# Kernel optimization log

Hardware: AMD Instinct MI355X
Metric: run time of the kernel (lower is better)

Reference implementation:

```python
import jax, jax.numpy as jnp
import numpy as np

B, T, D = 32, 1024, 512   # batch, encoder length, listener feature dim (= speller hidden)
H = 512                   # speller_hidden_dim
V = 64                    # output_class_dim
S = 128                   # max_label_len (decode steps, no teacher forcing)


def setup_inputs() -> dict:
    key = jax.random.key(0)
    ks = jax.random.split(key, 7)
    s = lambda n: 1.0 / np.sqrt(n)
    return {
        "listener_feature": jax.random.normal(ks[0], (B, T, D), jnp.float32),
        "W_ih": jax.random.normal(ks[1], (4 * H, V + H), jnp.float32) * s(V + H),
        "W_hh": jax.random.normal(ks[2], (4 * H, H), jnp.float32) * s(H),
        "b_ih": jax.random.normal(ks[3], (4 * H,), jnp.float32) * 0.01,
        "b_hh": jax.random.normal(ks[4], (4 * H,), jnp.float32) * 0.01,
        "W_out": jax.random.normal(ks[5], (V, 2 * H), jnp.float32) * s(2 * H),
        "b_out": jax.random.normal(ks[6], (V,), jnp.float32) * 0.01,
    }


def reference(listener_feature, W_ih, W_hh, b_ih, b_hh, W_out, b_out):
    Bb = listener_feature.shape[0]

    def step(carry, _):
        h, c, x = carry                              # h,c: [B,H]; x: [B,V+H]
        gates = x @ W_ih.T + b_ih + h @ W_hh.T + b_hh  # [B,4H], torch gate order i,f,g,o
        i, f, g, o = jnp.split(gates, 4, axis=-1)
        i = jax.nn.sigmoid(i); f = jax.nn.sigmoid(f)
        g = jnp.tanh(g);       o = jax.nn.sigmoid(o)
        c = f * c + i * g
        h = o * jnp.tanh(c)                          # rnn_output [B,H]
        # dot attention over listener features
        energy = jnp.einsum('bd,btd->bt', h, listener_feature)   # [B,T]
        attn = jax.nn.softmax(energy, axis=-1)
        ctx = jnp.einsum('bt,btd->bd', attn, listener_feature)   # [B,D]
        concat = jnp.concatenate([h, ctx], axis=-1)              # [B,2H]
        logp = jax.nn.log_softmax(concat @ W_out.T + b_out, axis=-1)  # [B,V]
        # decode_mode == 1: greedy one-hot feedback (non-differentiable argmax)
        ow = jax.nn.one_hot(jnp.argmax(logp, axis=-1), V, dtype=logp.dtype)
        x_next = jnp.concatenate([ow, ctx], axis=-1)
        return (h, c, x_next), (logp, attn)

    # initial word = one-hot of class 0; first rnn input concatenates listener_feature[:,0,:]
    ow0 = jnp.zeros((Bb, V), listener_feature.dtype).at[:, 0].set(1.0)
    x0 = jnp.concatenate([ow0, listener_feature[:, 0, :]], axis=-1)
    h0 = jnp.zeros((Bb, H), listener_feature.dtype)
    c0 = jnp.zeros((Bb, H), listener_feature.dtype)

    _, (raw_pred_seq, attention_record) = jax.lax.scan(step, (h0, c0, x0), None, length=S)
    return raw_pred_seq, attention_record   # [S,B,V], [S,B,T]
```

## Files before the change

### kernel.cpp

```cpp
#include <hip/hip_runtime.h>

#define Bn 32
#define Tn 1024
#define Dn 512
#define Hn 512
#define Vn 64
#define Sn 128
#define NTS 8
#define TT 128
#define NTHREADS 512
#define KIH 576
#define NBLK 256

#define LDS_BYTES 143360
#define OUT_ATT ((size_t)Sn * Bn * Vn)

#define WS_XCTX  1024
#define WS_XH    17408
#define WS_LGP   50176
#define WS_MST   66560
#define WS_LST   66816
#define WS_CTXP  67072

struct F8 { float4 a, b; };

__device__ __forceinline__ float bfu(unsigned short u){ return __uint_as_float(((unsigned int)u)<<16); }
__device__ __forceinline__ float bflo(unsigned int u){ return __uint_as_float(u<<16); }
__device__ __forceinline__ float bfhi(unsigned int u){ return __uint_as_float(u & 0xffff0000u); }
__device__ __forceinline__ unsigned short f2bf(float f){
  unsigned int x = __float_as_uint(f);
  return (unsigned short)((x + 0x7fffu + ((x>>16)&1u)) >> 16);
}
__device__ __forceinline__ F8 ld8(const unsigned short* p){
  uint4 q = *(const uint4*)p;
  F8 r;
  r.a = make_float4(bflo(q.x), bfhi(q.x), bflo(q.y), bfhi(q.y));
  r.b = make_float4(bflo(q.z), bfhi(q.z), bflo(q.w), bfhi(q.w));
  return r;
}
__device__ __forceinline__ F8 ld8(const float* p){
  F8 r; r.a = *(const float4*)p; r.b = *(const float4*)(p+4); return r;
}
__device__ __forceinline__ float dot8(F8 w, float4 a, float4 b){
  return w.a.x*a.x + w.a.y*a.y + w.a.z*a.z + w.a.w*a.w
       + w.b.x*b.x + w.b.y*b.y + w.b.z*b.z + w.b.w*b.w;
}
__device__ __forceinline__ float dot64g(const unsigned short* __restrict__ w, const float* x){
  const float4* x4 = (const float4*)x;
  float acc = 0.f;
#pragma unroll
  for(int i=0;i<8;i++) acc += dot8(ld8(w+8*i), x4[2*i], x4[2*i+1]);
  return acc;
}
__device__ __forceinline__ float sigm(float x){
  x = fminf(fmaxf(x, -30.f), 30.f); return 1.f/(1.f + expf(-x));
}
__device__ __forceinline__ float tnh(float x){
  return tanhf(fminf(fmaxf(x, -20.f), 20.f));
}

__device__ __forceinline__ void aput(float* p, float v){
  __hip_atomic_store(p, v, __ATOMIC_RELAXED, __HIP_MEMORY_SCOPE_AGENT);
}
__device__ __forceinline__ float aget(const float* p){
  return __hip_atomic_load(p, __ATOMIC_RELAXED, __HIP_MEMORY_SCOPE_AGENT);
}
__device__ __forceinline__ unsigned int uget(const unsigned int* p){
  return __hip_atomic_load(p, __ATOMIC_RELAXED, __HIP_MEMORY_SCOPE_AGENT);
}

__device__ __forceinline__ void gbar2(unsigned int* wsu, unsigned int ggen){
  asm volatile("s_waitcnt vmcnt(0)" ::: "memory");
  __syncthreads();
  const int tid = threadIdx.x;
  const int UP  = (int)blockIdx.x;
  const int grp = UP >> 3;
  if(UP == 0){
    if(tid < 64){
      if(tid == 0)
        __hip_atomic_fetch_add(&wsu[0], 1u, __ATOMIC_RELEASE, __HIP_MEMORY_SCOPE_AGENT);
      const unsigned int tgt = 8u*ggen;
      for(;;){
        unsigned int v = (tid < 32) ? uget(&wsu[tid*16]) : tgt;
        if(__all(v >= tgt)) break;
        __builtin_amdgcn_s_sleep(2);
      }
      if(tid == 0){
        __hip_atomic_store(&wsu[576], ggen, __ATOMIC_RELEASE, __HIP_MEMORY_SCOPE_AGENT);
        __hip_atomic_store(&wsu[8],   ggen, __ATOMIC_RELEASE, __HIP_MEMORY_SCOPE_AGENT);
        unsigned int x = __hip_atomic_load(&wsu[576], __ATOMIC_ACQUIRE, __HIP_MEMORY_SCOPE_AGENT);
        asm volatile("" :: "v"(x));
      }
    }
  } else if(tid == 0){
    __hip_atomic_fetch_add(&wsu[grp*16], 1u, __ATOMIC_RELEASE, __HIP_MEMORY_SCOPE_AGENT);
    if((UP & 7) == 0){
      while(uget(&wsu[576]) < ggen) __builtin_amdgcn_s_sleep(3);
      __hip_atomic_store(&wsu[grp*16 + 8], ggen, __ATOMIC_RELEASE, __HIP_MEMORY_SCOPE_AGENT);
    } else {
      while(uget(&wsu[grp*16 + 8]) < ggen) __builtin_amdgcn_s_sleep(3);
    }
    unsigned int x = __hip_atomic_load(&wsu[grp*16 + 8], __ATOMIC_ACQUIRE, __HIP_MEMORY_SCOPE_AGENT);
    asm volatile("" :: "v"(x));
  }
  __syncthreads();
  asm volatile("" ::: "memory");
}

__device__ __forceinline__ void gbarE(unsigned int* line){
  asm volatile("s_waitcnt vmcnt(0)" ::: "memory");
  __syncthreads();
  if(threadIdx.x == 0){
    unsigned int g = uget(line+1);
    unsigned int p = __hip_atomic_fetch_add(line, 1u, __ATOMIC_RELEASE, __HIP_MEMORY_SCOPE_AGENT);
    if(p == g*8u + 7u){
      __hip_atomic_store(line+1, g+1u, __ATOMIC_RELEASE, __HIP_MEMORY_SCOPE_AGENT);
    } else {
      while(uget(line+1) == g) __builtin_amdgcn_s_sleep(2);
    }
    unsigned int x = __hip_atomic_load(line+1, __ATOMIC_ACQUIRE, __HIP_MEMORY_SCOPE_AGENT);
    asm volatile("" :: "v"(x));
  }
  __syncthreads();
  asm volatile("" ::: "memory");
}

__global__ void dtype_probe(const unsigned short* __restrict__ b3, unsigned int* flag){
  const int t = threadIdx.x;
  bool ok = true;
#pragma unroll
  for(int i=0;i<8;i++){
    float v = bfu(b3[2*(t*8+i)]);
    ok = ok && (v == v) && (fabsf(v) < 0.5f);
  }
  unsigned long long m = __ballot(ok);
  if(t == 0)
    __hip_atomic_store(flag, (m == ~0ull) ? 1u : 2u, __ATOMIC_RELEASE, __HIP_MEMORY_SCOPE_AGENT);
}

__global__ __launch_bounds__(NTHREADS, 2)
void speller_v3(const float* __restrict__ lf,  const float* __restrict__ wih,
                const float* __restrict__ whh, const float* __restrict__ bih,
                const float* __restrict__ bhh, const float* __restrict__ wout,
                const float* __restrict__ bout, float* __restrict__ out,
                float* __restrict__ ws)
{
  { unsigned int fl = __hip_atomic_load((unsigned int*)ws + 512, __ATOMIC_ACQUIRE, __HIP_MEMORY_SCOPE_AGENT);
    if(fl != 2u) return; }

  const int tid   = threadIdx.x;
  const int UP    = (int)blockIdx.x;
  const int b_att = UP >> 3;
  const int ts    = UP & 7;
  const int w     = tid >> 6;
  const int lane  = tid & 63;

  extern __shared__ char smem[];
  float* tile   = (float*)smem;
  float* epart  = (float*)(smem + 131072);
  float* h_s    = epart + 512;
  float* e_s    = h_s + 512;
  float* p_s    = e_s + 128;
  float* red_s  = p_s + 128;
  float* pre_s  = red_s + 32;
  float* ctxc_s = pre_s + 256;
  float* c_s    = ctxc_s + 64;
  float* bias_s = c_s + 64;
  float* bout_s = bias_s + 8;
  int*   pall_s = (int*)(bout_s + 64);
  float* wow_s  = (float*)(pall_s + 32);

  unsigned int* wsu   = (unsigned int*)ws;
  unsigned int* eline = wsu + (size_t)b_att*16 + 4;
  float* xctx = ws + WS_XCTX;
  float* xh   = ws + WS_XH;
  float* lgp  = ws + WS_LGP;
  float* mst  = ws + WS_MST;
  float* lst  = ws + WS_LST;
  float* ctxp = ws + WS_CTXP;

  const int rw = (w>>1)*Hn + 2*UP + (w&1);

  float4 wv0, wv1, wv2, wv3;
  {
    const int k0 = 16*lane;
    const float* wp = (lane < 32) ? (wih + (size_t)rw*KIH + 64 + k0)
                                  : (whh + (size_t)rw*Hn + (k0 - 512));
    wv0 = *(const float4*)wp;     wv1 = *(const float4*)(wp+4);
    wv2 = *(const float4*)(wp+8); wv3 = *(const float4*)(wp+12);
  }
  float4 oh0, oh1, oc0, oc1;
  {
    const int v = tid>>3, q = tid&7;
    const float* pH = wout + (size_t)v*(2*Hn) + ts*64 + q*8;
    const float* pC = pH + Hn;
    oh0 = *(const float4*)pH; oh1 = *(const float4*)(pH+4);
    oc0 = *(const float4*)pC; oc1 = *(const float4*)(pC+4);
  }

  {
    const int rr = tid>>6, cc = tid&63;
    const int r2 = (rr>>1)*Hn + 2*UP + (rr&1);
    wow_s[tid] = wih[(size_t)r2*KIH + cc];
  }
  if(tid < 8){ const int r2 = (tid>>1)*Hn + 2*UP + (tid&1); bias_s[tid] = bih[r2] + bhh[r2]; }
  if(tid < Vn) bout_s[tid] = bout[tid];
  if(tid < 64) c_s[tid] = 0.f;
  if(tid < 32) pall_s[tid] = 0;

  float lfreg[64];
  {
    const float4* s4 = (const float4*)(lf + ((size_t)b_att*Tn + (size_t)ts*TT) * Dn);
    float4* d4 = (float4*)tile;
#pragma unroll
    for(int i=0;i<16;i++){
      const int f = tid + i*NTHREADS;
      const int row = f >> 7, cc = f & 127;
      d4[(row << 7) | (cc ^ (row & 7))] = s4[f];
    }
    const float* lfg = lf + ((size_t)b_att*Tn + (size_t)ts*TT + 64) * Dn + tid;
#pragma unroll
    for(int j=0;j<64;j++) lfreg[j] = lfg[(size_t)j*Dn];
  }

  if(tid < 64){
    aput(&xctx[(size_t)b_att*Dn + ts*64 + tid], lf[(size_t)b_att*Tn*Dn + ts*64 + tid]);
    const int bb = tid>>1, ul = tid&1;
    aput(&xh[(size_t)Bn*Hn + (size_t)bb*Hn + 2*UP + ul], 0.f);
  }
  __syncthreads();
  unsigned int gg = 0;
  gbar2(wsu, ++gg);

  for(int s = 0; s <= Sn; ++s){
    if(s > 0){
      for(int ii=0; ii<4; ++ii){
        const int bb = 4*w + ii;
        float lv = bout_s[lane];
        const float4* lp = (const float4*)(lgp + ((size_t)bb*Vn + lane)*8);
        float4 qa = lp[0], qb = lp[1];
        lv += qa.x+qa.y+qa.z+qa.w + qb.x+qb.y+qb.z+qb.w;
        float mv = lv; int mi = lane;
#pragma unroll
        for(int off=1; off<64; off<<=1){
          float ov = __shfl_xor(mv, off);
          int   oi = __shfl_xor(mi, off);
          if(ov > mv || (ov == mv && oi < mi)){ mv = ov; mi = oi; }
        }
        float se = expf(lv - mv);
#pragma unroll
        for(int off=1; off<64; off<<=1) se += __shfl_xor(se, off);
        if(lane == 0) pall_s[bb] = mi;
        if(UP == 8*bb) out[((size_t)(s-1)*Bn + bb)*Vn + lane] = lv - mv - logf(se);
      }
    }
    if(s == Sn) break;
    __syncthreads();

    {
      const float* xhR = xh + (size_t)(((s+1)&1))*Bn*Hn;
      const int k0 = 16*lane;
      for(int bb=0; bb<Bn; ++bb){
        const float* xp = (lane < 32) ? (xctx + (size_t)bb*Dn + k0)
                                      : (xhR  + (size_t)bb*Hn + (k0 - 512));
        float4 x0 = *(const float4*)xp,     x1 = *(const float4*)(xp+4),
               x2 = *(const float4*)(xp+8), x3 = *(const float4*)(xp+12);
        float acc = wv0.x*x0.x + wv0.y*x0.y + wv0.z*x0.z + wv0.w*x0.w
                  + wv1.x*x1.x + wv1.y*x1.y + wv1.z*x1.z + wv1.w*x1.w
                  + wv2.x*x2.x + wv2.y*x2.y + wv2.z*x2.z + wv2.w*x2.w
                  + wv3.x*x3.x + wv3.y*x3.y + wv3.z*x3.z + wv3.w*x3.w;
#pragma unroll
        for(int off=1; off<64; off<<=1) acc += __shfl_xor(acc, off);
        if(lane == 0) pre_s[w*Bn + bb] = acc;
      }
    }
    __syncthreads();
    if(tid < 64){
      const int bb = tid>>1, ul = tid&1;
      const int pidx = pall_s[bb];
      float gi = sigm(pre_s[(0+ul)*Bn+bb] + wow_s[(0+ul)*64+pidx] + bias_s[0+ul]);
      float gf = sigm(pre_s[(2+ul)*Bn+bb] + wow_s[(2+ul)*64+pidx] + bias_s[2+ul]);
      float gg2 = tnh(pre_s[(4+ul)*Bn+bb] + wow_s[(4+ul)*64+pidx] + bias_s[4+ul]);
      float go = sigm(pre_s[(6+ul)*Bn+bb] + wow_s[(6+ul)*64+pidx] + bias_s[6+ul]);
      float c = gf*c_s[tid] + gi*gg2;
      c_s[tid] = c;
      aput(&xh[(size_t)(s&1)*Bn*Hn + (size_t)bb*Hn + 2*UP + ul], go*tnh(c));
    }
    gbar2(wsu, ++gg);

    h_s[tid] = xh[(size_t)(s&1)*Bn*Hn + (size_t)b_att*Hn + tid];
    __syncthreads();
    {
      const int t1 = tid >> 3, q = tid & 7, mm = t1 & 7;
      const float4* lrow = (const float4*)tile + (size_t)t1*128;
      const float4* hq = (const float4*)(h_s + q*64);
      float ea = 0.f;
#pragma unroll
      for(int i=0;i<8;i++){
        const int c0 = q*16 + 2*i;
        F8 wv; wv.a = lrow[c0 ^ mm]; wv.b = lrow[(c0+1) ^ mm];
        ea += dot8(wv, hq[2*i], hq[2*i+1]);
      }
#pragma unroll
      for(int off=1; off<8; off<<=1) ea += __shfl_xor(ea, off);
      if(q==0) e_s[t1] = ea;
    }
    {
      const float h_own = h_s[tid];
      float mine = 0.f;
#pragma unroll
      for(int j=0;j<64;j++){
        float v = h_own * lfreg[j];
#pragma unroll
        for(int off=1; off<64; off<<=1) v += __shfl_xor(v, off);
        if(lane == j) mine = v;
      }
      epart[tid] = mine;
    }
    __syncthreads();
    if(tid < 64){
      float s2 = 0.f;
#pragma unroll
      for(int w2=0; w2<8; w2++) s2 += epart[(w2<<6) + tid];
      e_s[64 + tid] = s2;
      float v = fmaxf(e_s[tid], s2);
#pragma unroll
      for(int off=1; off<64; off<<=1) v = fmaxf(v, __shfl_xor(v,off));
      if(tid==0) red_s[10] = v;
    }
    __syncthreads();
    if(tid < TT) p_s[tid] = expf(e_s[tid] - red_s[10]);
    __syncthreads();
    if(tid < 64){
      float v = p_s[tid] + p_s[tid+64];
#pragma unroll
      for(int off=1; off<64; off<<=1) v += __shfl_xor(v,off);
      if(tid==0){
        aput(&mst[(size_t)b_att*NTS + ts], red_s[10]);
        aput(&lst[(size_t)b_att*NTS + ts], v);
      }
    }
    {
      float acc = 0.f;
      const int cs = tid >> 2, cr = tid & 3;
#pragma unroll
      for(int t=0;t<64;t++)
        acc += p_s[t] * tile[(size_t)t*Dn + (((cs ^ (t&7))<<2) | cr)];
#pragma unroll
      for(int j=0;j<64;j++) acc += p_s[64+j] * lfreg[j];
      aput(&ctxp[((size_t)b_att*NTS + ts)*Dn + tid], acc);
    }
    gbarE(eline);

    if(tid < NTS){
      red_s[16+tid] = mst[(size_t)b_att*NTS + tid];
      red_s[24+tid] = lst[(size_t)b_att*NTS + tid];
    }
    __syncthreads();
    if(tid == 0){
      float m = -3.0e38f;
#pragma unroll
      for(int j=0;j<NTS;j++) m = fmaxf(m, red_s[16+j]);
      float l = 0.f;
#pragma unroll
      for(int j=0;j<NTS;j++){ float fac = expf(red_s[16+j]-m); red_s[j]=fac; l += fac*red_s[24+j]; }
      red_s[8]=m; red_s[9]=l;
    }
    __syncthreads();
    {
      const float gm = red_s[8];
      const float gl = red_s[9];
      if(tid < TT)
        out[OUT_ATT + ((size_t)s*Bn + b_att)*Tn + (size_t)ts*TT + tid] = expf(e_s[tid] - gm)/gl;
      if(tid < 64){
        const int d = ts*64 + tid;
        float acc = 0.f;
#pragma unroll
        for(int j=0;j<NTS;j++) acc += red_s[j] * ctxp[((size_t)b_att*NTS + j)*Dn + d];
        const float cv = acc / gl;
        ctxc_s[tid] = cv;
        aput(&xctx[(size_t)b_att*Dn + d], cv);
      }
    }
    __syncthreads();
    {
      const int v = tid>>3, q = tid&7;
      const float4* hp = (const float4*)(h_s + ts*64 + q*8);
      const float4* cp = (const float4*)(ctxc_s + q*8);
      float4 ha = hp[0], hb = hp[1], ca = cp[0], cb = cp[1];
      float acc = oh0.x*ha.x + oh0.y*ha.y + oh0.z*ha.z + oh0.w*ha.w
                + oh1.x*hb.x + oh1.y*hb.y + oh1.z*hb.z + oh1.w*hb.w
                + oc0.x*ca.x + oc0.y*ca.y + oc0.z*ca.z + oc0.w*ca.w
                + oc1.x*cb.x + oc1.y*cb.y + oc1.z*cb.z + oc1.w*cb.w;
#pragma unroll
      for(int off=1; off<8; off<<=1) acc += __shfl_xor(acc, off);
      if(q == 0) aput(&lgp[((size_t)b_att*Vn + v)*8 + ts], acc);
    }
    gbar2(wsu, ++gg);
  }
}

__device__ __forceinline__ void gbar8(unsigned int* bar){
  asm volatile("s_waitcnt vmcnt(0)" ::: "memory");
  __syncthreads();
  if(threadIdx.x==0){
    unsigned int g = uget(bar+1);
    unsigned int p = __hip_atomic_fetch_add(bar, 1u, __ATOMIC_RELAXED, __HIP_MEMORY_SCOPE_AGENT);
    if(p == g*NTS + (NTS-1)){
      __hip_atomic_store(bar+1, g+1u, __ATOMIC_RELAXED, __HIP_MEMORY_SCOPE_AGENT);
    } else {
      while(uget(bar+1) == g) __builtin_amdgcn_s_sleep(2);
    }
  }
  __syncthreads();
  asm volatile("" ::: "memory");
}

__global__ __launch_bounds__(NTHREADS, 2)
void speller_bf16(const unsigned short* __restrict__ lf, const unsigned short* __restrict__ wih,
                  const unsigned short* __restrict__ whh, const unsigned short* __restrict__ bih,
                  const unsigned short* __restrict__ bhh, const unsigned short* __restrict__ wout,
                  const unsigned short* __restrict__ bout, unsigned short* __restrict__ out,
                  float* __restrict__ ws)
{
  { unsigned int fl = __hip_atomic_load((unsigned int*)ws + 512, __ATOMIC_ACQUIRE, __HIP_MEMORY_SCOPE_AGENT);
    if(fl != 1u) return; }
  const int tid = threadIdx.x;
  const int b   = (int)(blockIdx.x >> 3);
  const int ts  = (int)(blockIdx.x & 7);

  extern __shared__ char smem[];
  unsigned short* lf_s = (unsigned short*)smem;
  float* h_s   = (float*)(smem + 131072);
  float* ctx_s = h_s + 512;
  float* e_s   = ctx_s + 512;
  float* p_s   = e_s + 128;
  float* lg_s  = p_s + 128;
  float* red_s = lg_s + 64;
  float* c_s   = red_s + 32;
  int*   i_s   = (int*)(c_s + 64);

  unsigned int* bar = (unsigned int*)ws + (size_t)b*16 + 4;
  float* hbuf = ws + 1024  + (size_t)b*Hn;
  float* mstB = ws + WS_MST + (size_t)b*NTS;
  float* lstB = ws + WS_LST + (size_t)b*NTS;
  float* ctxpB= ws + WS_CTXP + (size_t)b*NTS*Dn;

  {
    const uint4* s4 = (const uint4*)(lf + ((size_t)b*Tn + (size_t)ts*TT) * Dn);
    uint4* d4 = (uint4*)lf_s;
#pragma unroll
    for(int i=0;i<16;i++) d4[tid + i*NTHREADS] = s4[tid + i*NTHREADS];
  }
  h_s[tid] = 0.f;
  if(tid < 64) c_s[tid] = 0.f;
  if(tid == 0) i_s[0] = 0;
  __syncthreads();

  for(int s = 0; s <= Sn; ++s){
    if(s > 0){
      if(tid < NTS){ red_s[16+tid] = aget(&mstB[tid]); red_s[24+tid] = aget(&lstB[tid]); }
      __syncthreads();
      if(tid == 0){
        float m = -3.0e38f;
#pragma unroll
        for(int j=0;j<NTS;j++) m = fmaxf(m, red_s[16+j]);
        float l = 0.f;
#pragma unroll
        for(int j=0;j<NTS;j++){ float fac = expf(red_s[16+j]-m); red_s[j]=fac; l += fac*red_s[24+j]; }
        red_s[8]=m; red_s[9]=l;
      }
      __syncthreads();
      const float gm = red_s[8];
      const float gl = red_s[9];
      {
        float acc = 0.f;
#pragma unroll
        for(int j=0;j<NTS;j++) acc += red_s[j] * aget(&ctxpB[(size_t)j*Dn + tid]);
        ctx_s[tid] = acc / gl;
      }
      if(tid < TT)
        out[OUT_ATT + ((size_t)(s-1)*Bn + b)*Tn + (size_t)ts*TT + tid] = f2bf(expf(e_s[tid]-gm)/gl);
      __syncthreads();
      {
        const int j = tid >> 3, ks = tid & 7;
        const unsigned short* wr = wout + (size_t)j*(2*Hn) + ks*128;
        float acc;
        if(ks < 4) acc = dot64g(wr, h_s + ks*128)       + dot64g(wr+64, h_s + ks*128 + 64);
        else       acc = dot64g(wr, ctx_s + (ks-4)*128) + dot64g(wr+64, ctx_s + (ks-4)*128 + 64);
#pragma unroll
        for(int off=1; off<8; off<<=1) acc += __shfl_xor(acc, off);
        if(ks==0) lg_s[j] = acc + bfu(bout[j]);
      }
      __syncthreads();
      if(tid < Vn){
        const float lv = lg_s[tid];
        float mv = lv; int mi = tid;
#pragma unroll
        for(int off=1; off<64; off<<=1){
          float ov = __shfl_xor(mv, off);
          int   oi = __shfl_xor(mi, off);
          if(ov > mv || (ov == mv && oi < mi)){ mv = ov; mi = oi; }
        }
        float se = expf(lv - mv);
#pragma unroll
        for(int off=1; off<64; off<<=1) se += __shfl_xor(se, off);
        if(ts == 0) out[((size_t)(s-1)*Bn + b)*Vn + tid] = f2bf(lv - mv - logf(se));
        if(tid == 0) i_s[0] = mi;
      }
      __syncthreads();
    } else {
      ctx_s[tid] = bfu(lf[(size_t)b*Tn*Dn + tid]);
      __syncthreads();
    }

    if(s == Sn) break;

    {
      const int u  = tid >> 3;
      const int ks = tid & 7;
      const int uu = ts*64 + u;
      const unsigned short* wi0 = wih + (size_t)(       uu)*KIH + 64 + ks*64;
      const unsigned short* wi1 = wih + (size_t)(  Hn + uu)*KIH + 64 + ks*64;
      const unsigned short* wi2 = wih + (size_t)(2*Hn + uu)*KIH + 64 + ks*64;
      const unsigned short* wi3 = wih + (size_t)(3*Hn + uu)*KIH + 64 + ks*64;
      const unsigned short* wh0 = whh + (size_t)(       uu)*Hn + ks*64;
      const unsigned short* wh1 = whh + (size_t)(  Hn + uu)*Hn + ks*64;
      const unsigned short* wh2 = whh + (size_t)(2*Hn + uu)*Hn + ks*64;
      const unsigned short* wh3 = whh + (size_t)(3*Hn + uu)*Hn + ks*64;
      const float4* xc = (const float4*)(ctx_s + ks*64);
      const float4* xh4 = (const float4*)(h_s   + ks*64);
      float a0=0.f,a1=0.f,a2=0.f,a3=0.f;
#pragma unroll
      for(int i=0;i<8;i++){
        float4 p0 = xc[2*i], p1 = xc[2*i+1];
        a0 += dot8(ld8(wi0+8*i), p0, p1);
        a1 += dot8(ld8(wi1+8*i), p0, p1);
        a2 += dot8(ld8(wi2+8*i), p0, p1);
        a3 += dot8(ld8(wi3+8*i), p0, p1);
      }
#pragma unroll
      for(int i=0;i<8;i++){
        float4 p0 = xh4[2*i], p1 = xh4[2*i+1];
        a0 += dot8(ld8(wh0+8*i), p0, p1);
        a1 += dot8(ld8(wh1+8*i), p0, p1);
        a2 += dot8(ld8(wh2+8*i), p0, p1);
        a3 += dot8(ld8(wh3+8*i), p0, p1);
      }
#pragma unroll
      for(int off=1; off<8; off<<=1){
        a0 += __shfl_xor(a0, off);
        a1 += __shfl_xor(a1, off);
        a2 += __shfl_xor(a2, off);
        a3 += __shfl_xor(a3, off);
      }
      if(ks == 0){
        const int pidx = i_s[0];
        const int r0 = uu, r1 = Hn+uu, r2 = 2*Hn+uu, r3 = 3*Hn+uu;
        float gi = a0 + bfu(wih[(size_t)r0*KIH + pidx]) + bfu(bih[r0]) + bfu(bhh[r0]);
        float gf = a1 + bfu(wih[(size_t)r1*KIH + pidx]) + bfu(bih[r1]) + bfu(bhh[r1]);
        float gg = a2 + bfu(wih[(size_t)r2*KIH + pidx]) + bfu(bih[r2]) + bfu(bhh[r2]);
        float go = a3 + bfu(wih[(size_t)r3*KIH + pidx]) + bfu(bih[r3]) + bfu(bhh[r3]);
        gi = sigm(gi); gf = sigm(gf); gg = tnh(gg); go = sigm(go);
        float c = gf*c_s[u] + gi*gg;
        c_s[u] = c;
        aput(&hbuf[uu], go * tnh(c));
      }
    }
    gbar8(bar);

    h_s[tid] = aget(&hbuf[tid]);
    __syncthreads();
    {
      const int t2 = tid >> 3;
      const int q  = tid & 7;
      const float4* hq = (const float4*)(h_s + q*64);
      float ea=0.f, eb=0.f;
      const unsigned short* la = lf_s + (size_t)(2*t2  )*Dn + q*64;
      const unsigned short* lb = lf_s + (size_t)(2*t2+1)*Dn + q*64;
#pragma unroll
      for(int i=0;i<8;i++){
        float4 p0 = hq[2*i], p1 = hq[2*i+1];
        ea += dot8(ld8(la+8*i), p0, p1);
        eb += dot8(ld8(lb+8*i), p0, p1);
      }
#pragma unroll
      for(int off=1; off<8; off<<=1){ ea += __shfl_xor(ea,off); eb += __shfl_xor(eb,off); }
      if(q==0){ e_s[2*t2] = ea; e_s[2*t2+1] = eb; }
    }
    __syncthreads();
    if(tid < 64){
      float v = fmaxf(e_s[tid], e_s[tid+64]);
#pragma unroll
      for(int off=1; off<64; off<<=1) v = fmaxf(v, __shfl_xor(v,off));
      if(tid==0) red_s[10] = v;
    }
    __syncthreads();
    if(tid < TT) p_s[tid] = expf(e_s[tid] - red_s[10]);
    __syncthreads();
    if(tid < 64){
      float v = p_s[tid] + p_s[tid+64];
#pragma unroll
      for(int off=1; off<64; off<<=1) v += __shfl_xor(v,off);
      if(tid==0){ aput(&mstB[ts], red_s[10]); aput(&lstB[ts], v); }
    }
    {
      float acc = 0.f;
      const unsigned short* col = lf_s + tid;
#pragma unroll 4
      for(int t=0;t<TT;t++) acc += p_s[t] * bfu(col[(size_t)t*Dn]);
      aput(&ctxpB[(size_t)ts*Dn + tid], acc);
    }
    gbar8(bar);
  }
}

extern "C" void kernel_launch(void* const* d_in, const int* in_sizes, int n_in,
                              void* d_out, int out_size, void* d_ws, size_t ws_size,
                              hipStream_t stream) {
  (void)in_sizes; (void)n_in; (void)out_size; (void)ws_size;
  float* ws = (float*)d_ws;

  hipFuncSetAttribute(reinterpret_cast<const void*>(&speller_v3),
                      hipFuncAttributeMaxDynamicSharedMemorySize, LDS_BYTES);
  hipFuncSetAttribute(reinterpret_cast<const void*>(&speller_bf16),
                      hipFuncAttributeMaxDynamicSharedMemorySize, LDS_BYTES);
  hipMemsetAsync(d_ws, 0, 4096, stream);
  dtype_probe<<<dim3(1), dim3(64), 0, stream>>>((const unsigned short*)d_in[3],
                                                (unsigned int*)d_ws + 512);
  speller_v3<<<dim3(NBLK), dim3(NTHREADS), LDS_BYTES, stream>>>(
      (const float*)d_in[0], (const float*)d_in[1], (const float*)d_in[2],
      (const float*)d_in[3], (const float*)d_in[4], (const float*)d_in[5],
      (const float*)d_in[6], (float*)d_out, ws);
  speller_bf16<<<dim3(NBLK), dim3(NTHREADS), LDS_BYTES, stream>>>(
      (const unsigned short*)d_in[0], (const unsigned short*)d_in[1],
      (const unsigned short*)d_in[2], (const unsigned short*)d_in[3],
      (const unsigned short*)d_in[4], (const unsigned short*)d_in[5],
      (const unsigned short*)d_in[6], (unsigned short*)d_out, ws);
}
```

Measured before the change: 8.282 ms.

## Use butterfly reduce-scatter for wave reductions and flatten grid barrier

Replaces the per-batch full-wave shuffle reductions in the gate pre-activation and attention-energy loops with a recursive-halving reduce-scatter. Each lane now ends up holding one of the 32 sums, which cuts the shuffle count from about 6×N to about N. The grid barrier is also flattened: block 0 releases all group flags directly instead of going through group leaders, and sleep intervals are shortened. Launch bounds drop to one block per SM, which frees registers for the 32-entry accumulator arrays but gives up the occupancy hint.

Result: faster. 6.769 ms (-18.3%).

```diff
diff --git a/kernel.cpp b/kernel.cpp
--- a/kernel.cpp
+++ b/kernel.cpp
@@ -59,6 +59,25 @@
   return tanhf(fminf(fmaxf(x, -20.f), 20.f));
 }
 
+template<int N>
+__device__ __forceinline__ void rs_round(float* a, int off, bool hi){
+#pragma unroll
+  for(int i=0;i<N;i++){
+    float send = hi ? a[i]   : a[i+N];
+    float keep = hi ? a[i+N] : a[i];
+    float recv = __shfl_xor(send, off);
+    a[i] = keep + recv;
+  }
+}
+__device__ __forceinline__ void rs32(float* a, int lane){
+  rs_round<16>(a, 32, (lane&32)!=0);
+  rs_round< 8>(a, 16, (lane&16)!=0);
+  rs_round< 4>(a,  8, (lane& 8)!=0);
+  rs_round< 2>(a,  4, (lane& 4)!=0);
+  rs_round< 1>(a,  2, (lane& 2)!=0);
+  a[0] += __shfl_xor(a[0], 1);
+}
+
 __device__ __forceinline__ void aput(float* p, float v){
   __hip_atomic_store(p, v, __ATOMIC_RELAXED, __HIP_MEMORY_SCOPE_AGENT);
 }
@@ -83,23 +102,16 @@
       for(;;){
         unsigned int v = (tid < 32) ? uget(&wsu[tid*16]) : tgt;
         if(__all(v >= tgt)) break;
-        __builtin_amdgcn_s_sleep(2);
-      }
-      if(tid == 0){
-        __hip_atomic_store(&wsu[576], ggen, __ATOMIC_RELEASE, __HIP_MEMORY_SCOPE_AGENT);
-        __hip_atomic_store(&wsu[8],   ggen, __ATOMIC_RELEASE, __HIP_MEMORY_SCOPE_AGENT);
-        unsigned int x = __hip_atomic_load(&wsu[576], __ATOMIC_ACQUIRE, __HIP_MEMORY_SCOPE_AGENT);
-        asm volatile("" :: "v"(x));
-      }
+        __builtin_amdgcn_s_sleep(1);
+      }
+      if(tid < 32)
+        __hip_atomic_store(&wsu[tid*16 + 8], ggen, __ATOMIC_RELEASE, __HIP_MEMORY_SCOPE_AGENT);
     }
   } else if(tid == 0){
     __hip_atomic_fetch_add(&wsu[grp*16], 1u, __ATOMIC_RELEASE, __HIP_MEMORY_SCOPE_AGENT);
-    if((UP & 7) == 0){
-      while(uget(&wsu[576]) < ggen) __builtin_amdgcn_s_sleep(3);
-      __hip_atomic_store(&wsu[grp*16 + 8], ggen, __ATOMIC_RELEASE, __HIP_MEMORY_SCOPE_AGENT);
-    } else {
-      while(uget(&wsu[grp*16 + 8]) < ggen) __builtin_amdgcn_s_sleep(3);
-    }
+    while(uget(&wsu[grp*16 + 8]) < ggen) __builtin_amdgcn_s_sleep(1);
+  }
+  if(tid == 0){
     unsigned int x = __hip_atomic_load(&wsu[grp*16 + 8], __ATOMIC_ACQUIRE, __HIP_MEMORY_SCOPE_AGENT);
     asm volatile("" :: "v"(x));
   }
@@ -116,7 +128,7 @@
     if(p == g*8u + 7u){
       __hip_atomic_store(line+1, g+1u, __ATOMIC_RELEASE, __HIP_MEMORY_SCOPE_AGENT);
     } else {
-      while(uget(line+1) == g) __builtin_amdgcn_s_sleep(2);
+      while(uget(line+1) == g) __builtin_amdgcn_s_sleep(1);
     }
     unsigned int x = __hip_atomic_load(line+1, __ATOMIC_ACQUIRE, __HIP_MEMORY_SCOPE_AGENT);
     asm volatile("" :: "v"(x));
@@ -138,7 +150,7 @@
     __hip_atomic_store(flag, (m == ~0ull) ? 1u : 2u, __ATOMIC_RELEASE, __HIP_MEMORY_SCOPE_AGENT);
 }
 
-__global__ __launch_bounds__(NTHREADS, 2)
+__global__ __launch_bounds__(NTHREADS, 1)
 void speller_v3(const float* __restrict__ lf,  const float* __restrict__ wih,
                 const float* __restrict__ whh, const float* __restrict__ bih,
                 const float* __restrict__ bhh, const float* __restrict__ wout,
@@ -260,19 +272,19 @@
     {
       const float* xhR = xh + (size_t)(((s+1)&1))*Bn*Hn;
       const int k0 = 16*lane;
+      const float* xbase = (lane < 32) ? (xctx + k0) : (xhR + (k0 - 512));
+      float acc[Bn];
+#pragma unroll
       for(int bb=0; bb<Bn; ++bb){
-        const float* xp = (lane < 32) ? (xctx + (size_t)bb*Dn + k0)
-                                      : (xhR  + (size_t)bb*Hn + (k0 - 512));
-        float4 x0 = *(const float4*)xp,     x1 = *(const float4*)(xp+4),
-               x2 = *(const float4*)(xp+8), x3 = *(const float4*)(xp+12);
-        float acc = wv0.x*x0.x + wv0.y*x0.y + wv0.z*x0.z + wv0.w*x0.w
-                  + wv1.x*x1.x + wv1.y*x1.y + wv1.z*x1.z + wv1.w*x1.w
-                  + wv2.x*x2.x + wv2.y*x2.y + wv2.z*x2.z + wv2.w*x2.w
-                  + wv3.x*x3.x + wv3.y*x3.y + wv3.z*x3.z + wv3.w*x3.w;
-#pragma unroll
-        for(int off=1; off<64; off<<=1) acc += __shfl_xor(acc, off);
-        if(lane == 0) pre_s[w*Bn + bb] = acc;
-      }
+        const float4* xp = (const float4*)(xbase + (size_t)bb*Dn);
+        float4 x0 = xp[0], x1 = xp[1], x2 = xp[2], x3 = xp[3];
+        acc[bb] = wv0.x*x0.x + wv0.y*x0.y + wv0.z*x0.z + wv0.w*x0.w
+                + wv1.x*x1.x + wv1.y*x1.y + wv1.z*x1.z + wv1.w*x1.w
+                + wv2.x*x2.x + wv2.y*x2.y + wv2.z*x2.z + wv2.w*x2.w
+                + wv3.x*x3.x + wv3.y*x3.y + wv3.z*x3.z + wv3.w*x3.w;
+      }
+      rs32(acc, lane);
+      if((lane & 1) == 0) pre_s[w*Bn + (lane>>1)] = acc[0];
     }
     __syncthreads();
     if(tid < 64){
@@ -307,15 +319,15 @@
     }
     {
       const float h_own = h_s[tid];
-      float mine = 0.f;
-#pragma unroll
-      for(int j=0;j<64;j++){
-        float v = h_own * lfreg[j];
-#pragma unroll
-        for(int off=1; off<64; off<<=1) v += __shfl_xor(v, off);
-        if(lane == j) mine = v;
-      }
-      epart[tid] = mine;
+      float a[32];
+#pragma unroll
+      for(int j=0;j<32;j++) a[j] = h_own * lfreg[j];
+      rs32(a, lane);
+      if((lane & 1) == 0) epart[(w<<6) + (lane>>1)] = a[0];
+#pragma unroll
+      for(int j=0;j<32;j++) a[j] = h_own * lfreg[32+j];
+      rs32(a, lane);
+      if((lane & 1) == 0) epart[(w<<6) + 32 + (lane>>1)] = a[0];
     }
     __syncthreads();
     if(tid < 64){
```
